# Kernel optimization log

Hardware: AMD Instinct MI355X
Metric: run time of the kernel (lower is better)

## Reference

```python
import jax, jax.numpy as jnp
import numpy as np

B, CIN, H, W = 16, 256, 48, 48
K, CD, MULTI = 64, 64, 1
GAMMA = (1.0 - 1e-10) ** (1.0 ** 0.6)  # iter = 1


def _ln(v, s, b, eps=1e-5):
    m = v.mean(-1, keepdims=True)
    var = ((v - m) ** 2).mean(-1, keepdims=True)
    return (v - m) / jnp.sqrt(var + eps) * s + b


def _spatial_masks():
    # pairwise squared distance between (i,j) grid coords, N = H*W
    ii, jj = jnp.meshgrid(jnp.arange(H, dtype=jnp.float32), jnp.arange(W, dtype=jnp.float32), indexing='ij')
    coord = jnp.stack([ii.ravel(), jj.ravel()], axis=1)  # [N,2]
    sq = (coord ** 2).sum(-1, keepdims=True)             # [N,1]
    d2 = sq - 2.0 * (coord @ coord.T) + sq.T             # [N,N]
    m = jnp.exp(-jnp.sqrt(jnp.abs(d2)))
    A = m / m.sum(0, keepdims=True)  # column-normalized (torch sums dim=1 of [B,N,N])
    cur, out = A, []
    for _ in range(MULTI):
        cur = cur @ A  # A^(num+2)
        out.append(cur)
    return out


def setup_inputs() -> dict:
    key = jax.random.key(0)
    ks = jax.random.split(key, 3)
    x = jax.random.normal(ks[0], (B, CIN, H, W), jnp.float32)
    clusters = jax.random.normal(ks[1], (1, K, CD), jnp.float32) * 0.1
    pi = jnp.ones((1, K), jnp.float32) / K
    cov = jnp.ones((1, K), jnp.float32)
    w_proj = jax.random.normal(ks[2], (CD, CIN), jnp.float32) / np.sqrt(CIN)
    nt_scale = jnp.ones((CD,), jnp.float32)
    nt_bias = jnp.zeros((CD,), jnp.float32)
    pn_scale = jnp.ones((K * MULTI,), jnp.float32)
    pn_bias = jnp.zeros((K * MULTI,), jnp.float32)
    return dict(x=x, clusters=clusters, pi=pi, cov=cov, w_proj=w_proj,
                nt_scale=nt_scale, nt_bias=nt_bias, pn_scale=pn_scale, pn_bias=pn_bias)


def reference(x, clusters, pi, cov, w_proj, nt_scale, nt_bias, pn_scale, pn_bias):
    N = H * W
    # 1x1 conv projection -> tokens [B,N,CD]
    xf = jnp.einsum('bihw,ci->bhwc', x, w_proj).reshape(B, N, CD)
    # normalized templates (batch-invariant)
    t = _ln(clusters[0], nt_scale, nt_bias)  # [K,CD]
    # squared euclidean distance via expansion (avoids [B,CD,N,K] intermediate)
    x2 = (xf ** 2).sum(-1)  # [B,N]
    t2 = (t ** 2).sum(-1)   # [K]
    d = x2[:, :, None] + t2[None, None, :] - 2.0 * jnp.einsum('bnc,kc->bnk', xf, t)
    logits = jnp.log(pi[0] / jnp.sqrt(cov[0])) - d / cov[0] / 2.0
    attn = jax.nn.softmax(logits, axis=-1)  # [B,N,K]
    # EM-style updates
    pi_new = pi + GAMMA * (attn.sum(1) / N - pi)                     # [B,K]
    attn_n = attn + 1e-8
    attn_n = attn_n / attn_n.sum(-2, keepdims=True)                  # normalize over N
    t_new = clusters + GAMMA * (jnp.einsum('bnc,bnk->bkc', xf, attn_n) - clusters)  # [B,K,CD]
    tn2 = (t_new ** 2).sum(-1)  # [B,K]
    d2 = x2[:, :, None] + tn2[:, None, :] - 2.0 * jnp.einsum('bnc,bkc->bnk', xf, t_new)
    cov_new = cov + GAMMA * ((d2 * attn_n).sum(1) - cov)             # [B,K]
    # spatial distance-encoding masks (stop-gradient / constant w.r.t. params)
    masks = _spatial_masks()
    outp = jnp.concatenate([jnp.einsum('bnk,nm->bkm', attn_n, M) for M in masks], axis=1)  # [B,K*MULTI,N]
    outp = _ln(outp.transpose(0, 2, 1), pn_scale, pn_bias).transpose(0, 2, 1)
    outp = outp.reshape(B, K * MULTI, H, W)
    attn_out = attn.transpose(0, 2, 1).reshape(B, K, H, W)
    return outp, attn_out, t_new, pi_new, cov_new
```

## Files before the change

kernel.cpp:

```cpp
#include <hip/hip_runtime.h>
#include <hip/hip_bf16.h>
#include <math.h>

#define B_   16
#define CIN_ 256
#define H_   48
#define W_   48
#define N_   2304
#define K_   64
#define CD_  64

#define GAMMA_F 0.9999999999f

using f32x4  = __attribute__((ext_vector_type(4))) float;
using bf16x8 = __attribute__((ext_vector_type(8))) short;
using s16x4  = __attribute__((ext_vector_type(4))) short;

__device__ __forceinline__ void split_bf(float x, short& hi, short& lo) {
  unsigned u = __builtin_bit_cast(unsigned, x);
  unsigned r = (u + 0x7FFFu + ((u >> 16) & 1u)) & 0xFFFF0000u;
  hi = (short)(r >> 16);
  float res = x - __builtin_bit_cast(float, r);
  unsigned u2 = __builtin_bit_cast(unsigned, res);
  unsigned r2 = u2 + 0x7FFFu + ((u2 >> 16) & 1u);
  lo = (short)(r2 >> 16);
}

constexpr size_t OFF_XF    = 0;
constexpr size_t OFF_ANT   = OFF_XF    + (size_t)B_*N_*CD_;
constexpr size_t OFF_T     = OFF_ANT   + (size_t)B_*K_*N_;
constexpr size_t OFF_T2    = OFF_T     + (size_t)K_*CD_;
constexpr size_t OFF_LOGPI = OFF_T2    + K_;
constexpr size_t OFF_I2C   = OFF_LOGPI + K_;
constexpr size_t OFF_X2    = OFF_I2C   + K_;
constexpr size_t OFF_CS    = OFF_X2    + (size_t)B_*N_;
constexpr size_t OFF_ICN   = OFF_CS    + (size_t)B_*K_;
constexpr size_t OFF_MASKH = OFF_ICN   + (size_t)B_*K_;
constexpr size_t OFF_MASKL = OFF_MASKH + (size_t)N_*N_/2;

constexpr size_t OUT_OUTP = 0;
constexpr size_t OUT_ATTN = (size_t)B_*K_*N_;
constexpr size_t OUT_TNEW = OUT_ATTN + (size_t)B_*K_*N_;
constexpr size_t OUT_PI   = OUT_TNEW + (size_t)B_*K_*CD_;
constexpr size_t OUT_COV  = OUT_PI   + (size_t)B_*K_;

__global__ __launch_bounds__(256) void k_proj(const float* __restrict__ x, const float* __restrict__ wp,
                                              float* __restrict__ xf) {
  __shared__ float xs[32][64];
  __shared__ float ws_[32][65];
  int b = blockIdx.y, n0 = blockIdx.x * 64;
  int tid = threadIdx.x;
  int nn = tid & 63, cg = tid >> 6;
  float acc[16];
#pragma unroll
  for (int j = 0; j < 16; j++) acc[j] = 0.f;
  for (int i0 = 0; i0 < CIN_; i0 += 32) {
#pragma unroll
    for (int j = 0; j < 8; j++) {
      int ii = cg * 8 + j;
      xs[ii][nn] = x[((size_t)b * CIN_ + i0 + ii) * N_ + n0 + nn];
    }
    {
      int c = tid >> 2, iq = (tid & 3) * 8;
#pragma unroll
      for (int j = 0; j < 8; j++)
        ws_[iq + j][c] = wp[(size_t)c * CIN_ + i0 + iq + j];
    }
    __syncthreads();
#pragma unroll
    for (int ii = 0; ii < 32; ++ii) {
      float xv = xs[ii][nn];
#pragma unroll
      for (int j = 0; j < 16; j++) acc[j] += xv * ws_[ii][cg * 16 + j];
    }
    __syncthreads();
  }
  float* dst = xf + ((size_t)b * N_ + n0 + nn) * CD_ + cg * 16;
#pragma unroll
  for (int j4 = 0; j4 < 4; j4++)
    *(float4*)(dst + j4 * 4) = make_float4(acc[j4*4], acc[j4*4+1], acc[j4*4+2], acc[j4*4+3]);
}

__global__ void k_templ(const float* __restrict__ clusters, const float* __restrict__ pi,
                        const float* __restrict__ cov, const float* __restrict__ nsc,
                        const float* __restrict__ nbi, float* __restrict__ t, float* __restrict__ t2,
                        float* __restrict__ logpi, float* __restrict__ i2c) {
  int k = threadIdx.x;
  float v[CD_];
  float m = 0;
#pragma unroll
  for (int c = 0; c < CD_; c++) { v[c] = clusters[k * CD_ + c]; m += v[c]; }
  m /= CD_;
  float var = 0;
#pragma unroll
  for (int c = 0; c < CD_; c++) { float d = v[c] - m; var += d * d; }
  var /= CD_;
  float inv = 1.f / sqrtf(var + 1e-5f);
  float s2 = 0;
#pragma unroll
  for (int c = 0; c < CD_; c++) {
    float tv = (v[c] - m) * inv * nsc[c] + nbi[c];
    t[k * CD_ + c] = tv;
    s2 += tv * tv;
  }
  t2[k] = s2;
  float p = pi[k], cv = cov[k];
  logpi[k] = logf(p) - 0.5f * logf(cv);
  i2c[k] = 0.5f / cv;
}

__global__ __launch_bounds__(256) void k_attn(const float* __restrict__ xf, const float* __restrict__ t,
                                              const float* __restrict__ t2, const float* __restrict__ logpi,
                                              const float* __restrict__ i2c,
                                              float* __restrict__ aout, float* __restrict__ x2o) {
  __shared__ __align__(16) float ts[K_][72];
  __shared__ float t2s[K_], lps[K_], ics[K_];
  int tid = threadIdx.x;
  for (int i = tid; i < K_ * CD_; i += 256) ts[i >> 6][i & 63] = t[i];
  if (tid < K_) { t2s[tid] = t2[tid]; lps[tid] = logpi[tid]; ics[tid] = i2c[tid]; }
  __syncthreads();
  int b = blockIdx.y;
  int tok = tid >> 2, kg = tid & 3;
  int n = blockIdx.x * 64 + tok;
  const float4* xr = (const float4*)(xf + ((size_t)b * N_ + n) * CD_);
  float4 xv[16];
#pragma unroll
  for (int i = 0; i < 16; i++) xv[i] = xr[i];
  float x2 = 0;
#pragma unroll
  for (int i = 0; i < 16; i++) x2 += xv[i].x * xv[i].x + xv[i].y * xv[i].y + xv[i].z * xv[i].z + xv[i].w * xv[i].w;
  if (kg == 0) x2o[(size_t)b * N_ + n] = x2;
  float lg[16];
#pragma unroll
  for (int kk = 0; kk < 16; kk++) {
    int k = kk * 4 + kg;
    const float4* tk = (const float4*)&ts[k][0];
    float dot = 0;
#pragma unroll
    for (int i = 0; i < 16; i++) {
      float4 tv = tk[i];
      dot += xv[i].x * tv.x + xv[i].y * tv.y + xv[i].z * tv.z + xv[i].w * tv.w;
    }
    lg[kk] = lps[k] - (x2 + t2s[k] - 2.f * dot) * ics[k];
  }
  float mx = lg[0];
#pragma unroll
  for (int kk = 1; kk < 16; kk++) mx = fmaxf(mx, lg[kk]);
  mx = fmaxf(mx, __shfl_xor(mx, 1));
  mx = fmaxf(mx, __shfl_xor(mx, 2));
  float sum = 0;
#pragma unroll
  for (int kk = 0; kk < 16; kk++) { lg[kk] = __expf(lg[kk] - mx); sum += lg[kk]; }
  sum += __shfl_xor(sum, 1);
  sum += __shfl_xor(sum, 2);
  float inv = 1.f / sum;
  size_t base = (size_t)b * K_ * N_ + n;
#pragma unroll
  for (int kk = 0; kk < 16; kk++)
    aout[base + (size_t)(kk * 4 + kg) * N_] = lg[kk] * inv;
}

__global__ __launch_bounds__(256) void k_colsum2(const float* __restrict__ ant, float* __restrict__ colsum) {
  int r = blockIdx.x, tid = threadIdx.x;
  const float* row = ant + (size_t)r * N_;
  float s = 0;
  for (int n = tid; n < N_; n += 256) s += row[n];
#pragma unroll
  for (int off = 32; off; off >>= 1) s += __shfl_down(s, off);
  __shared__ float red[4];
  if ((tid & 63) == 0) red[tid >> 6] = s;
  __syncthreads();
  if (tid == 0) colsum[r] = red[0] + red[1] + red[2] + red[3];
}

__global__ void k_pinew(const float* __restrict__ colsum, const float* __restrict__ pi,
                        float* __restrict__ pi_out, float* __restrict__ icn) {
  int b = blockIdx.x, k = threadIdx.x;
  float cs = colsum[b * K_ + k];
  float p = pi[k];
  pi_out[b * K_ + k] = p + GAMMA_F * (cs / (float)N_ - p);
  icn[b * K_ + k] = 1.f / (cs + (float)N_ * 1e-8f);
}

__global__ __launch_bounds__(256) void k_tnew_cov(const float* __restrict__ ant, const float* __restrict__ icn,
                                                  const float* __restrict__ xf, const float* __restrict__ x2,
                                                  const float* __restrict__ clusters, const float* __restrict__ cov,
                                                  float* __restrict__ tnew_out, float* __restrict__ cov_out) {
  int k = blockIdx.x, b = blockIdx.y;
  int tid = threadIdx.x;
  int c = tid & 63, g = tid >> 6;
  const float* arow = ant + ((size_t)b * K_ + k) * N_;
  const float* x2r = x2 + (size_t)b * N_;
  float acc = 0, ax2 = 0;
#pragma unroll 4
  for (int n = g; n < N_; n += 4) {
    float a = arow[n] + 1e-8f;
    acc += a * xf[((size_t)b * N_ + n) * CD_ + c];
    ax2 += a * x2r[n];
  }
  __shared__ float red[4][64];
  __shared__ float red2[4];
  red[g][c] = acc;
  if (c == 0) red2[g] = ax2;
  __syncthreads();
  if (tid < 64) {
    float icnv = icn[b * K_ + k];
    float s = (red[0][c] + red[1][c] + red[2][c] + red[3][c]) * icnv;
    float cl = clusters[k * CD_ + c];
    float tv = cl + GAMMA_F * (s - cl);
    tnew_out[((size_t)b * K_ + k) * CD_ + c] = tv;
    float sq = tv * tv;
    float st = s * tv;
#pragma unroll
    for (int off = 32; off; off >>= 1) { sq += __shfl_down(sq, off); st += __shfl_down(st, off); }
    if (c == 0) {
      float ax2t = (red2[0] + red2[1] + red2[2] + red2[3]) * icnv;
      float cv = cov[k];
      float csum = ax2t + sq - 2.f * st;
      cov_out[b * K_ + k] = cv + GAMMA_F * (csum - cv);
    }
  }
}

__global__ __launch_bounds__(256) void k_amean(const float* __restrict__ ant, const float* __restrict__ icn,
                                               float* __restrict__ amean) {
  int b = blockIdx.y;
  int n = blockIdx.x * 256 + threadIdx.x;
  const float* base = ant + (size_t)b * K_ * N_ + n;
  const float* ic = icn + b * K_;
  float s = 0;
#pragma unroll 8
  for (int k = 0; k < K_; k++)
    s += (base[(size_t)k * N_] + 1e-8f) * ic[k];
  amean[(size_t)b * N_ + n] = s * (1.f / (float)K_);
}

__global__ __launch_bounds__(256) void k_mask(short* __restrict__ MH, short* __restrict__ ML) {
  __shared__ float red[4];
  const int m = blockIdx.x;
  const int mi = m / W_, mj = m % W_;
  const int tid = threadIdx.x;
  float e[N_ / 256];
  float s = 0;
#pragma unroll
  for (int it = 0; it < N_ / 256; it++) {
    int n = it * 256 + tid;
    int ni = n / W_, nj = n - (n / W_) * W_;
    int dx = ni - mi, dy = nj - mj;
    e[it] = __expf(-sqrtf((float)(dx * dx + dy * dy)));
    s += e[it];
  }
#pragma unroll
  for (int off = 32; off; off >>= 1) s += __shfl_down(s, off);
  if ((tid & 63) == 0) red[tid >> 6] = s;
  __syncthreads();
  const float imc = 1.f / (red[0] + red[1] + red[2] + red[3]);
#pragma unroll
  for (int it = 0; it < N_ / 256; it++) {
    int n = it * 256 + tid;
    short h, l;
    split_bf(e[it] * imc, h, l);
    MH[(size_t)m * N_ + n] = h;
    ML[(size_t)m * N_ + n] = l;
  }
}


__global__ __launch_bounds__(256) void gemm1_mfma(const float* __restrict__ Am, const float* __restrict__ icn,
                                                  const float* __restrict__ amean,
                                                  const short* __restrict__ MaskH, const short* __restrict__ MaskL,
                                                  short* __restrict__ YdH, short* __restrict__ YdL) {
  __shared__ __align__(16) short Ah[64][40];
  __shared__ __align__(16) short Al[64][40];
  __shared__ __align__(16) short Bh[64][40];
  __shared__ __align__(16) short Bl[64][40];
  const int tid = threadIdx.x;
  const int b = blockIdx.y;
  const int m0 = b * 64, n0 = blockIdx.x * 64;
  const int lane = tid & 63, w = tid >> 6;
  const int fr = lane & 15, quad = lane >> 4;
  const int srow = tid >> 2;
  const int skq  = (tid & 3) * 8;
  const float ic = icn[m0 + srow];
  const float badd = 1e-8f * ic;
  const size_t mrow = (size_t)(n0 + srow) * N_;
  f32x4 acc[4] = {};
  for (int k0 = 0; k0 < N_; k0 += 32) {
    const float* ap = Am + (size_t)(m0 + srow) * N_ + k0 + skq;
    const float* mp = amean + (size_t)b * N_ + k0 + skq;
    float va[8];
    {
      float4 a0 = *(const float4*)ap;
      float4 a1 = *(const float4*)(ap + 4);
      float4 u0 = *(const float4*)mp;
      float4 u1 = *(const float4*)(mp + 4);
      va[0] = fmaf(a0.x, ic, badd) - u0.x; va[1] = fmaf(a0.y, ic, badd) - u0.y;
      va[2] = fmaf(a0.z, ic, badd) - u0.z; va[3] = fmaf(a0.w, ic, badd) - u0.w;
      va[4] = fmaf(a1.x, ic, badd) - u1.x; va[5] = fmaf(a1.y, ic, badd) - u1.y;
      va[6] = fmaf(a1.z, ic, badd) - u1.z; va[7] = fmaf(a1.w, ic, badd) - u1.w;
    }
    bf16x8 avh, avl;
#pragma unroll
    for (int j = 0; j < 8; j++) { short h, l; split_bf(va[j], h, l); avh[j] = h; avl[j] = l; }
    *(bf16x8*)&Ah[srow][skq] = avh;
    *(bf16x8*)&Al[srow][skq] = avl;
    *(bf16x8*)&Bh[srow][skq] = *(const bf16x8*)&MaskH[mrow + k0 + skq];
    *(bf16x8*)&Bl[srow][skq] = *(const bf16x8*)&MaskL[mrow + k0 + skq];
    __syncthreads();
    bf16x8 afh = *(const bf16x8*)&Ah[w * 16 + fr][quad * 8];
    bf16x8 afl = *(const bf16x8*)&Al[w * 16 + fr][quad * 8];
#pragma unroll
    for (int ns = 0; ns < 4; ns++) {
      bf16x8 bfh = *(const bf16x8*)&Bh[ns * 16 + fr][quad * 8];
      bf16x8 bfl = *(const bf16x8*)&Bl[ns * 16 + fr][quad * 8];
      acc[ns] = __builtin_amdgcn_mfma_f32_16x16x32_bf16(afh, bfh, acc[ns], 0, 0, 0);
      acc[ns] = __builtin_amdgcn_mfma_f32_16x16x32_bf16(afh, bfl, acc[ns], 0, 0, 0);
      acc[ns] = __builtin_amdgcn_mfma_f32_16x16x32_bf16(afl, bfh, acc[ns], 0, 0, 0);
    }
    __syncthreads();
  }
  const size_t rbase = (size_t)(m0 + w * 16 + fr) * N_ + n0;
#pragma unroll
  for (int ns = 0; ns < 4; ns++) {
    s16x4 h4, l4;
#pragma unroll
    for (int reg = 0; reg < 4; reg++) { short h, l; split_bf(acc[ns][reg], h, l); h4[reg] = h; l4[reg] = l; }
    *(s16x4*)&YdH[rbase + ns * 16 + quad * 4] = h4;
    *(s16x4*)&YdL[rbase + ns * 16 + quad * 4] = l4;
  }
}

__global__ __launch_bounds__(256) void gemm2_ln_mfma(const short* __restrict__ YdH, const short* __restrict__ YdL,
                                                     const short* __restrict__ MaskH, const short* __restrict__ MaskL,
                                                     const float* __restrict__ pns, const float* __restrict__ pnb,
                                                     float* __restrict__ outp) {
  __shared__ __align__(16) short Ah[64][40];
  __shared__ __align__(16) short Al[64][40];
  __shared__ __align__(16) short Bh[64][40];
  __shared__ __align__(16) short Bl[64][40];
  __shared__ __align__(16) float S[64][68];
  __shared__ float rstd[64], sc[64], bi[64];
  const int tid = threadIdx.x;
  const int b = blockIdx.y;
  const int m0 = b * 64, n0 = blockIdx.x * 64;
  const int lane = tid & 63, w = tid >> 6;
  const int fr = lane & 15, quad = lane >> 4;
  const int srow = tid >> 2;
  const int skq  = (tid & 3) * 8;
  const size_t mrow = (size_t)(n0 + srow) * N_;
  if (tid < 64) { sc[tid] = pns[tid]; bi[tid] = pnb[tid]; }
  f32x4 acc[4] = {};
  for (int k0 = 0; k0 < N_; k0 += 32) {
    const size_t aoff = (size_t)(m0 + srow) * N_ + k0 + skq;
    *(bf16x8*)&Ah[srow][skq] = *(const bf16x8*)&YdH[aoff];
    *(bf16x8*)&Al[srow][skq] = *(const bf16x8*)&YdL[aoff];
    *(bf16x8*)&Bh[srow][skq] = *(const bf16x8*)&MaskH[mrow + k0 + skq];
    *(bf16x8*)&Bl[srow][skq] = *(const bf16x8*)&MaskL[mrow + k0 + skq];
    __syncthreads();
    bf16x8 afh = *(const bf16x8*)&Ah[w * 16 + fr][quad * 8];
    bf16x8 afl = *(const bf16x8*)&Al[w * 16 + fr][quad * 8];
#pragma unroll
    for (int ns = 0; ns < 4; ns++) {
      bf16x8 bfh = *(const bf16x8*)&Bh[ns * 16 + fr][quad * 8];
      bf16x8 bfl = *(const bf16x8*)&Bl[ns * 16 + fr][quad * 8];
      acc[ns] = __builtin_amdgcn_mfma_f32_16x16x32_bf16(afh, bfh, acc[ns], 0, 0, 0);
      acc[ns] = __builtin_amdgcn_mfma_f32_16x16x32_bf16(afh, bfl, acc[ns], 0, 0, 0);
      acc[ns] = __builtin_amdgcn_mfma_f32_16x16x32_bf16(afl, bfh, acc[ns], 0, 0, 0);
    }
    __syncthreads();
  }
#pragma unroll
  for (int ns = 0; ns < 4; ns++)
    *(f32x4*)&S[w * 16 + fr][ns * 16 + quad * 4] = acc[ns];
  __syncthreads();
  if (tid < 64) {
    float ss = 0;
#pragma unroll
    for (int k = 0; k < K_; k++) { float d = S[k][tid]; ss += d * d; }
    rstd[tid] = 1.f / sqrtf(ss / (float)K_ + 1e-5f);
  }
  __syncthreads();
  {
    int c = tid & 63, g = tid >> 6;
#pragma unroll
    for (int i = 0; i < 16; i++) {
      int r = g * 16 + i;
      outp[(size_t)(m0 + r) * N_ + n0 + c] = S[r][c] * rstd[c] * sc[r] + bi[r];
    }
  }
}

extern "C" void kernel_launch(void* const* d_in, const int* in_sizes, int n_in,
                              void* d_out, int out_size, void* d_ws, size_t ws_size,
                              hipStream_t stream) {
  const float* x        = (const float*)d_in[0];
  const float* clusters = (const float*)d_in[1];
  const float* pi       = (const float*)d_in[2];
  const float* cov      = (const float*)d_in[3];
  const float* w_proj   = (const float*)d_in[4];
  const float* nt_scale = (const float*)d_in[5];
  const float* nt_bias  = (const float*)d_in[6];
  const float* pn_scale = (const float*)d_in[7];
  const float* pn_bias  = (const float*)d_in[8];
  float* out = (float*)d_out;
  float* w = (float*)d_ws;
  short* YdH = (short*)(w + OFF_XF);
  short* YdL = YdH + (size_t)B_ * K_ * N_;
  short* MaskH = (short*)(w + OFF_MASKH);
  short* MaskL = (short*)(w + OFF_MASKL);
  float* attn = out + OUT_ATTN;

  k_mask<<<N_, 256, 0, stream>>>(MaskH, MaskL);
  k_proj<<<dim3(N_ / 64, B_), 256, 0, stream>>>(x, w_proj, w + OFF_XF);
  k_templ<<<1, K_, 0, stream>>>(clusters, pi, cov, nt_scale, nt_bias,
                                w + OFF_T, w + OFF_T2, w + OFF_LOGPI, w + OFF_I2C);
  k_attn<<<dim3(N_ / 64, B_), 256, 0, stream>>>(w + OFF_XF, w + OFF_T, w + OFF_T2,
                                                w + OFF_LOGPI, w + OFF_I2C,
                                                attn, w + OFF_X2);
  k_colsum2<<<B_ * K_, 256, 0, stream>>>(attn, w + OFF_CS);
  k_pinew<<<B_, K_, 0, stream>>>(w + OFF_CS, pi, out + OUT_PI, w + OFF_ICN);
  k_tnew_cov<<<dim3(K_, B_), 256, 0, stream>>>(attn, w + OFF_ICN, w + OFF_XF, w + OFF_X2,
                                               clusters, cov, out + OUT_TNEW, out + OUT_COV);
  k_amean<<<dim3(N_ / 256, B_), 256, 0, stream>>>(attn, w + OFF_ICN, w + OFF_X2);
  gemm1_mfma<<<dim3(N_ / 64, B_), 256, 0, stream>>>(attn, w + OFF_ICN, w + OFF_X2,
                                                    MaskH, MaskL, YdH, YdL);
  gemm2_ln_mfma<<<dim3(N_ / 64, B_), 256, 0, stream>>>(YdH, YdL, MaskH, MaskL,
                                                       pn_scale, pn_bias, out + OUT_OUTP);
}
```

Baseline: 418.7 us.

## Double-buffer LDS tiles and prefetch next K-slice in mask GEMMs

Both mask GEMM kernels now use two LDS buffers and register-prefetch the next 32-wide K slice of the A and mask operands while MFMAs run on the current one. This drops one barrier per iteration and hides global load latency behind compute. The logits kernel's dot product is also split into four independent accumulators to break the serial add chain. The cost is doubled shared memory per block, which may reduce occupancy, and a slightly different summation order in the dot product.

```diff
diff --git a/kernel.cpp b/kernel.cpp
--- a/kernel.cpp
+++ b/kernel.cpp
@@ -135,12 +135,16 @@
   for (int kk = 0; kk < 16; kk++) {
     int k = kk * 4 + kg;
     const float4* tk = (const float4*)&ts[k][0];
-    float dot = 0;
-#pragma unroll
-    for (int i = 0; i < 16; i++) {
-      float4 tv = tk[i];
-      dot += xv[i].x * tv.x + xv[i].y * tv.y + xv[i].z * tv.z + xv[i].w * tv.w;
-    }
+    float d0 = 0, d1 = 0, d2 = 0, d3 = 0;
+#pragma unroll
+    for (int i = 0; i < 16; i += 4) {
+      float4 t0 = tk[i], t1 = tk[i + 1], t2v = tk[i + 2], t3 = tk[i + 3];
+      d0 += xv[i].x * t0.x + xv[i].y * t0.y + xv[i].z * t0.z + xv[i].w * t0.w;
+      d1 += xv[i+1].x * t1.x + xv[i+1].y * t1.y + xv[i+1].z * t1.z + xv[i+1].w * t1.w;
+      d2 += xv[i+2].x * t2v.x + xv[i+2].y * t2v.y + xv[i+2].z * t2v.z + xv[i+2].w * t2v.w;
+      d3 += xv[i+3].x * t3.x + xv[i+3].y * t3.y + xv[i+3].z * t3.z + xv[i+3].w * t3.w;
+    }
+    float dot = (d0 + d1) + (d2 + d3);
     lg[kk] = lps[k] - (x2 + t2s[k] - 2.f * dot) * ics[k];
   }
   float mx = lg[0];
@@ -270,10 +274,10 @@
                                                   const float* __restrict__ amean,
                                                   const short* __restrict__ MaskH, const short* __restrict__ MaskL,
                                                   short* __restrict__ YdH, short* __restrict__ YdL) {
-  __shared__ __align__(16) short Ah[64][40];
-  __shared__ __align__(16) short Al[64][40];
-  __shared__ __align__(16) short Bh[64][40];
-  __shared__ __align__(16) short Bl[64][40];
+  __shared__ __align__(16) short Ah[2][64][40];
+  __shared__ __align__(16) short Al[2][64][40];
+  __shared__ __align__(16) short Bh[2][64][40];
+  __shared__ __align__(16) short Bl[2][64][40];
   const int tid = threadIdx.x;
   const int b = blockIdx.y;
   const int m0 = b * 64, n0 = blockIdx.x * 64;
@@ -284,40 +288,48 @@
   const float ic = icn[m0 + srow];
   const float badd = 1e-8f * ic;
   const size_t mrow = (size_t)(n0 + srow) * N_;
+  const float* apb = Am + (size_t)(m0 + srow) * N_ + skq;
+  const float* mpb = amean + (size_t)b * N_ + skq;
   f32x4 acc[4] = {};
+  float4 a0 = *(const float4*)apb;
+  float4 a1 = *(const float4*)(apb + 4);
+  float4 u0 = *(const float4*)mpb;
+  float4 u1 = *(const float4*)(mpb + 4);
+  bf16x8 mh = *(const bf16x8*)&MaskH[mrow + skq];
+  bf16x8 ml = *(const bf16x8*)&MaskL[mrow + skq];
   for (int k0 = 0; k0 < N_; k0 += 32) {
-    const float* ap = Am + (size_t)(m0 + srow) * N_ + k0 + skq;
-    const float* mp = amean + (size_t)b * N_ + k0 + skq;
+    const int c = (k0 >> 5) & 1;
     float va[8];
-    {
-      float4 a0 = *(const float4*)ap;
-      float4 a1 = *(const float4*)(ap + 4);
-      float4 u0 = *(const float4*)mp;
-      float4 u1 = *(const float4*)(mp + 4);
-      va[0] = fmaf(a0.x, ic, badd) - u0.x; va[1] = fmaf(a0.y, ic, badd) - u0.y;
-      va[2] = fmaf(a0.z, ic, badd) - u0.z; va[3] = fmaf(a0.w, ic, badd) - u0.w;
-      va[4] = fmaf(a1.x, ic, badd) - u1.x; va[5] = fmaf(a1.y, ic, badd) - u1.y;
-      va[6] = fmaf(a1.z, ic, badd) - u1.z; va[7] = fmaf(a1.w, ic, badd) - u1.w;
-    }
+    va[0] = fmaf(a0.x, ic, badd) - u0.x; va[1] = fmaf(a0.y, ic, badd) - u0.y;
+    va[2] = fmaf(a0.z, ic, badd) - u0.z; va[3] = fmaf(a0.w, ic, badd) - u0.w;
+    va[4] = fmaf(a1.x, ic, badd) - u1.x; va[5] = fmaf(a1.y, ic, badd) - u1.y;
+    va[6] = fmaf(a1.z, ic, badd) - u1.z; va[7] = fmaf(a1.w, ic, badd) - u1.w;
     bf16x8 avh, avl;
 #pragma unroll
     for (int j = 0; j < 8; j++) { short h, l; split_bf(va[j], h, l); avh[j] = h; avl[j] = l; }
-    *(bf16x8*)&Ah[srow][skq] = avh;
-    *(bf16x8*)&Al[srow][skq] = avl;
-    *(bf16x8*)&Bh[srow][skq] = *(const bf16x8*)&MaskH[mrow + k0 + skq];
-    *(bf16x8*)&Bl[srow][skq] = *(const bf16x8*)&MaskL[mrow + k0 + skq];
+    *(bf16x8*)&Ah[c][srow][skq] = avh;
+    *(bf16x8*)&Al[c][srow][skq] = avl;
+    *(bf16x8*)&Bh[c][srow][skq] = mh;
+    *(bf16x8*)&Bl[c][srow][skq] = ml;
+    if (k0 + 32 < N_) {
+      a0 = *(const float4*)(apb + k0 + 32);
+      a1 = *(const float4*)(apb + k0 + 36);
+      u0 = *(const float4*)(mpb + k0 + 32);
+      u1 = *(const float4*)(mpb + k0 + 36);
+      mh = *(const bf16x8*)&MaskH[mrow + k0 + 32 + skq];
+      ml = *(const bf16x8*)&MaskL[mrow + k0 + 32 + skq];
+    }
     __syncthreads();
-    bf16x8 afh = *(const bf16x8*)&Ah[w * 16 + fr][quad * 8];
-    bf16x8 afl = *(const bf16x8*)&Al[w * 16 + fr][quad * 8];
+    bf16x8 afh = *(const bf16x8*)&Ah[c][w * 16 + fr][quad * 8];
+    bf16x8 afl = *(const bf16x8*)&Al[c][w * 16 + fr][quad * 8];
 #pragma unroll
     for (int ns = 0; ns < 4; ns++) {
-      bf16x8 bfh = *(const bf16x8*)&Bh[ns * 16 + fr][quad * 8];
-      bf16x8 bfl = *(const bf16x8*)&Bl[ns * 16 + fr][quad * 8];
+      bf16x8 bfh = *(const bf16x8*)&Bh[c][ns * 16 + fr][quad * 8];
+      bf16x8 bfl = *(const bf16x8*)&Bl[c][ns * 16 + fr][quad * 8];
       acc[ns] = __builtin_amdgcn_mfma_f32_16x16x32_bf16(afh, bfh, acc[ns], 0, 0, 0);
       acc[ns] = __builtin_amdgcn_mfma_f32_16x16x32_bf16(afh, bfl, acc[ns], 0, 0, 0);
       acc[ns] = __builtin_amdgcn_mfma_f32_16x16x32_bf16(afl, bfh, acc[ns], 0, 0, 0);
     }
-    __syncthreads();
   }
   const size_t rbase = (size_t)(m0 + w * 16 + fr) * N_ + n0;
 #pragma unroll
@@ -334,10 +346,10 @@
                                                      const short* __restrict__ MaskH, const short* __restrict__ MaskL,
                                                      const float* __restrict__ pns, const float* __restrict__ pnb,
                                                      float* __restrict__ outp) {
-  __shared__ __align__(16) short Ah[64][40];
-  __shared__ __align__(16) short Al[64][40];
-  __shared__ __align__(16) short Bh[64][40];
-  __shared__ __align__(16) short Bl[64][40];
+  __shared__ __align__(16) short Ah[2][64][40];
+  __shared__ __align__(16) short Al[2][64][40];
+  __shared__ __align__(16) short Bh[2][64][40];
+  __shared__ __align__(16) short Bl[2][64][40];
   __shared__ __align__(16) float S[64][68];
   __shared__ float rstd[64], sc[64], bi[64];
   const int tid = threadIdx.x;
@@ -349,26 +361,37 @@
   const int skq  = (tid & 3) * 8;
   const size_t mrow = (size_t)(n0 + srow) * N_;
   if (tid < 64) { sc[tid] = pns[tid]; bi[tid] = pnb[tid]; }
+  const size_t abase = (size_t)(m0 + srow) * N_ + skq;
   f32x4 acc[4] = {};
+  bf16x8 yh = *(const bf16x8*)&YdH[abase];
+  bf16x8 yl = *(const bf16x8*)&YdL[abase];
+  bf16x8 mh = *(const bf16x8*)&MaskH[mrow + skq];
+  bf16x8 ml = *(const bf16x8*)&MaskL[mrow + skq];
   for (int k0 = 0; k0 < N_; k0 += 32) {
-    const size_t aoff = (size_t)(m0 + srow) * N_ + k0 + skq;
-    *(bf16x8*)&Ah[srow][skq] = *(const bf16x8*)&YdH[aoff];
-    *(bf16x8*)&Al[srow][skq] = *(const bf16x8*)&YdL[aoff];
-    *(bf16x8*)&Bh[srow][skq] = *(const bf16x8*)&MaskH[mrow + k0 + skq];
-    *(bf16x8*)&Bl[srow][skq] = *(const bf16x8*)&MaskL[mrow + k0 + skq];
+    const int c = (k0 >> 5) & 1;
+    *(bf16x8*)&Ah[c][srow][skq] = yh;
+    *(bf16x8*)&Al[c][srow][skq] = yl;
+    *(bf16x8*)&Bh[c][srow][skq] = mh;
+    *(bf16x8*)&Bl[c][srow][skq] = ml;
+    if (k0 + 32 < N_) {
+      yh = *(const bf16x8*)&YdH[abase + k0 + 32];
+      yl = *(const bf16x8*)&YdL[abase + k0 + 32];
+      mh = *(const bf16x8*)&MaskH[mrow + k0 + 32 + skq];
+      ml = *(const bf16x8*)&MaskL[mrow + k0 + 32 + skq];
+    }
     __syncthreads();
-    bf16x8 afh = *(const bf16x8*)&Ah[w * 16 + fr][quad * 8];
-    bf16x8 afl = *(const bf16x8*)&Al[w * 16 + fr][quad * 8];
+    bf16x8 afh = *(const bf16x8*)&Ah[c][w * 16 + fr][quad * 8];
+    bf16x8 afl = *(const bf16x8*)&Al[c][w * 16 + fr][quad * 8];
 #pragma unroll
     for (int ns = 0; ns < 4; ns++) {
-      bf16x8 bfh = *(const bf16x8*)&Bh[ns * 16 + fr][quad * 8];
-      bf16x8 bfl = *(const bf16x8*)&Bl[ns * 16 + fr][quad * 8];
+      bf16x8 bfh = *(const bf16x8*)&Bh[c][ns * 16 + fr][quad * 8];
+      bf16x8 bfl = *(const bf16x8*)&Bl[c][ns * 16 + fr][quad * 8];
       acc[ns] = __builtin_amdgcn_mfma_f32_16x16x32_bf16(afh, bfh, acc[ns], 0, 0, 0);
       acc[ns] = __builtin_amdgcn_mfma_f32_16x16x32_bf16(afh, bfl, acc[ns], 0, 0, 0);
       acc[ns] = __builtin_amdgcn_mfma_f32_16x16x32_bf16(afl, bfh, acc[ns], 0, 0, 0);
     }
-    __syncthreads();
-  }
+  }
+  __syncthreads();
 #pragma unroll
   for (int ns = 0; ns < 4; ns++)
     *(f32x4*)&S[w * 16 + fr][ns * 16 + quad * 4] = acc[ns];
```

Measured after the change: 377.5 us. 1.11x faster.
